# Performance work log

Hardware: AMD Instinct MI355X
Metric: run time of the kernel (lower is better)

The kernel has to match this reference:

```python
import jax, jax.numpy as jnp
import numpy as np
import math

NUM_HEADS = 16
ATTN_WIDTH = 256


def setup_inputs() -> dict:
    key = jax.random.key(0)
    ks = jax.random.split(key, 5)
    B, S, C, H = 2, 2048, 1024, 1024
    scale = 0.02
    return {
        "x": jax.random.normal(ks[0], (B, S, C), dtype=jnp.float32),
        "Wq": jax.random.normal(ks[1], (C, H), dtype=jnp.float32) * scale,
        "Wk": jax.random.normal(ks[2], (C, H), dtype=jnp.float32) * scale,
        "Wv": jax.random.normal(ks[3], (C, H), dtype=jnp.float32) * scale,
        "Wo": jax.random.normal(ks[4], (H, C), dtype=jnp.float32) * scale,
    }


def reference(x, Wq, Wk, Wv, Wo):
    B, S, C = x.shape
    H = NUM_HEADS
    dh = Wq.shape[1] // H  # head dim; Q.size(-1) in torch code

    def split_heads(t):
        # [B, S, H*dh] -> [B, H, S, dh]
        return t.reshape(B, S, H, dh).transpose(0, 2, 1, 3)

    q = split_heads(x @ Wq)
    k = split_heads(x @ Wk)
    v = split_heads(x @ Wv)

    scores = jnp.einsum("bhqd,bhkd->bhqk", q, k) / math.sqrt(dh)
    # exp-shift (first 'softmax-like' step, unnormalized)
    scores = jnp.exp(scores - jnp.max(scores, axis=-1, keepdims=True))
    # banded mask: tril(attn_width//2 - 1).triu(-(attn_width//2))
    i = jnp.arange(S)[:, None]
    j = jnp.arange(S)[None, :]
    d = j - i
    half = ATTN_WIDTH // 2
    mask = (d <= half - 1) & (d >= -half)
    scores = jnp.where(mask, scores, 0.0)
    # second softmax over the masked exp-scores (zeros contribute exp(0)=1)
    weights = jax.nn.softmax(scores, axis=-1)

    out = jnp.einsum("bhqk,bhkd->bhqd", weights, v)  # [B, H, S, dh]
    out = out.transpose(0, 2, 1, 3).reshape(B, S, H * dh)
    return out @ Wo
```

## Files before the change

kernel.cpp:

```cpp
#include <hip/hip_runtime.h>
#include <math.h>

typedef __bf16 bf16_t;
typedef bf16_t bf16x8 __attribute__((ext_vector_type(8)));
typedef bf16_t bf16x4 __attribute__((ext_vector_type(4)));
typedef float f32x4 __attribute__((ext_vector_type(4)));

constexpr int S_ = 2048;
constexpr float SCALE = 0.125f;

#define MFMA_B16(a, b, c) __builtin_amdgcn_mfma_f32_16x16x32_bf16(a, b, c, 0, 0, 0)

#define WAIT_VM0() __builtin_amdgcn_s_waitcnt(0x0F70)
#define WAIT_VM4() __builtin_amdgcn_s_waitcnt(0x0F74)
#define WAIT_VM8() __builtin_amdgcn_s_waitcnt(0x0F78)
#define BARRIER()  __builtin_amdgcn_s_barrier()

typedef __attribute__((address_space(1))) const void* as1_cvp;
typedef __attribute__((address_space(3))) void* as3_vp;

__device__ __forceinline__ void gl2lds16(const void* g, void* l)
{
    __builtin_amdgcn_global_load_lds((as1_cvp)g, (as3_vp)l, 16, 0, 0);
}

__global__ __launch_bounds__(256) void prep(const float* __restrict__ x,
                                            const float* __restrict__ Wq,
                                            const float* __restrict__ Wk,
                                            const float* __restrict__ Wv,
                                            const float* __restrict__ Wo,
                                            bf16_t* __restrict__ xb,
                                            bf16_t* __restrict__ Wqt,
                                            bf16_t* __restrict__ Wkt,
                                            bf16_t* __restrict__ Wvt,
                                            bf16_t* __restrict__ Wot,
                                            float* __restrict__ vsp)
{
    __shared__ float T[64][65];
    const int blk = blockIdx.x;
    const int tid = threadIdx.x;
    if (blk < 1024) {
#pragma unroll
        for (int u = 0; u < 4; ++u) {
            const int g = blk * 1024 + u * 256 + tid;
            const float4 v = ((const float4*)x)[g];
            bf16x4 o;
            o[0] = (bf16_t)v.x; o[1] = (bf16_t)v.y;
            o[2] = (bf16_t)v.z; o[3] = (bf16_t)v.w;
            *(bf16x4*)&xb[(size_t)g * 4] = o;
        }
    } else if (blk < 2048) {
        const int rem = blk - 1024;
        const int wsel = rem >> 8, t = rem & 255;
        const float* src = (wsel == 0) ? Wq : (wsel == 1) ? Wk : (wsel == 2) ? Wv : Wo;
        bf16_t* dst = (wsel == 0) ? Wqt : (wsel == 1) ? Wkt : (wsel == 2) ? Wvt : Wot;
        const int k0 = (t >> 4) * 64, n0 = (t & 15) * 64;
        const int rr = tid >> 4, c4 = (tid & 15) * 4;
#pragma unroll
        for (int u = 0; u < 4; ++u) {
            const float4 v = *(const float4*)&src[(size_t)(k0 + u * 16 + rr) * 1024 + n0 + c4];
            T[u * 16 + rr][c4 + 0] = v.x; T[u * 16 + rr][c4 + 1] = v.y;
            T[u * 16 + rr][c4 + 2] = v.z; T[u * 16 + rr][c4 + 3] = v.w;
        }
        __syncthreads();
#pragma unroll
        for (int u = 0; u < 4; ++u) {
            bf16x4 o;
#pragma unroll
            for (int e = 0; e < 4; ++e) o[e] = (bf16_t)T[c4 + e][u * 16 + rr];
            *(bf16x4*)&dst[(size_t)(n0 + u * 16 + rr) * 1024 + k0 + c4] = o;
        }
    } else {
#pragma unroll
        for (int u = 0; u < 8; ++u) vsp[u * 256 + tid] = 0.f;
    }
}

template <int MODE>
__device__ __forceinline__ void mfma_gemm_body(const bf16_t* __restrict__ A,
                                               const bf16_t* __restrict__ Bt,
                                               void* __restrict__ dst,
                                               float* __restrict__ vsum_out,
                                               int m0, int n0)
{
    __shared__ bf16_t As[12288];
    __shared__ bf16_t Bs[12288];

    const int tid = threadIdx.x;
    const int lane = tid & 63, wid = tid >> 6;
    const int l15 = lane & 15, quad = lane >> 4;
    const int wm = (wid & 1) * 64, wn = (wid >> 1) * 64;

    const int srow = wid * 32 + (lane >> 2);
    const int scg8 = (lane & 3) * 8;
    const bf16_t* Ag0 = A  + (size_t)(m0 + srow) * 1024 + scg8;
    const bf16_t* Ag1 = A  + (size_t)(m0 + srow + 16) * 1024 + scg8;
    const bf16_t* Bg0 = Bt + (size_t)(n0 + srow) * 1024 + scg8;
    const bf16_t* Bg1 = Bt + (size_t)(n0 + srow + 16) * 1024 + scg8;

    f32x4 acc[4][4];
#pragma unroll
    for (int i = 0; i < 4; ++i)
#pragma unroll
        for (int j = 0; j < 4; ++j) acc[i][j] = (f32x4){0.f, 0.f, 0.f, 0.f};

#pragma unroll
    for (int p = 0; p < 2; ++p) {
        const int k0 = p * 32;
        gl2lds16(Ag0 + k0, As + p * 4096 + (wid * 2 + 0) * 512);
        gl2lds16(Ag1 + k0, As + p * 4096 + (wid * 2 + 1) * 512);
        gl2lds16(Bg0 + k0, Bs + p * 4096 + (wid * 2 + 0) * 512);
        gl2lds16(Bg1 + k0, Bs + p * 4096 + (wid * 2 + 1) * 512);
    }

    int cbuf = 0, sbuf = 2;
    for (int it = 0; it < 32; ++it) {
        if (it + 2 < 32) WAIT_VM4(); else WAIT_VM0();
        BARRIER();
        if (it + 2 < 32) {
            const int k0 = (it + 2) * 32;
            gl2lds16(Ag0 + k0, As + sbuf * 4096 + (wid * 2 + 0) * 512);
            gl2lds16(Ag1 + k0, As + sbuf * 4096 + (wid * 2 + 1) * 512);
            gl2lds16(Bg0 + k0, Bs + sbuf * 4096 + (wid * 2 + 0) * 512);
            gl2lds16(Bg1 + k0, Bs + sbuf * 4096 + (wid * 2 + 1) * 512);
            sbuf = (sbuf == 2) ? 0 : sbuf + 1;
        }
        bf16x8 af[4], bfr[4];
#pragma unroll
        for (int mt = 0; mt < 4; ++mt)
            af[mt] = *(const bf16x8*)&As[cbuf * 4096 + (wm + mt * 16 + l15) * 32 + quad * 8];
#pragma unroll
        for (int nt = 0; nt < 4; ++nt)
            bfr[nt] = *(const bf16x8*)&Bs[cbuf * 4096 + (wn + nt * 16 + l15) * 32 + quad * 8];
#pragma unroll
        for (int mt = 0; mt < 4; ++mt)
#pragma unroll
            for (int nt = 0; nt < 4; ++nt)
                acc[mt][nt] = MFMA_B16(bfr[nt], af[mt], acc[mt][nt]);
        cbuf = (cbuf == 2) ? 0 : cbuf + 1;
    }

#pragma unroll
    for (int mt = 0; mt < 4; ++mt) {
        const int m = m0 + wm + mt * 16 + l15;
#pragma unroll
        for (int nt = 0; nt < 4; ++nt) {
            const int nb = n0 + wn + nt * 16 + quad * 4;
            if (MODE == 0) {
                *(f32x4*)&((float*)dst)[(size_t)m * 1024 + nb] = acc[mt][nt];
            } else {
                const int bb = m >> 11, s = m & 2047;
                const int hh = nb >> 6, d = nb & 63;
                bf16x4 o;
#pragma unroll
                for (int u = 0; u < 4; ++u) o[u] = (bf16_t)acc[mt][nt][u];
                *(bf16x4*)&((bf16_t*)dst)[((size_t)(bb * 16 + hh) * 2048 + s) * 64 + d] = o;
            }
        }
    }

    if (MODE == 1 && vsum_out != nullptr) {
        const int bb = m0 >> 11;
#pragma unroll
        for (int nt = 0; nt < 4; ++nt) {
            f32x4 p = acc[0][nt];
#pragma unroll
            for (int mt = 1; mt < 4; ++mt) {
                p[0] += acc[mt][nt][0]; p[1] += acc[mt][nt][1];
                p[2] += acc[mt][nt][2]; p[3] += acc[mt][nt][3];
            }
#pragma unroll
            for (int st = 1; st < 16; st <<= 1) {
                p[0] += __shfl_xor(p[0], st);
                p[1] += __shfl_xor(p[1], st);
                p[2] += __shfl_xor(p[2], st);
                p[3] += __shfl_xor(p[3], st);
            }
            if (l15 == 0) {
                const int nI = n0 + wn + nt * 16 + quad * 4;
                float* vp = &vsum_out[(bb * 16 + (nI >> 6)) * 64 + (nI & 63)];
                atomicAdd(vp + 0, p[0]);
                atomicAdd(vp + 1, p[1]);
                atomicAdd(vp + 2, p[2]);
                atomicAdd(vp + 3, p[3]);
            }
        }
    }
}

__global__ __launch_bounds__(256) void gemm_qkv_mfma(const bf16_t* __restrict__ xb,
                                                     const bf16_t* __restrict__ Wqt,
                                                     const bf16_t* __restrict__ Wkt,
                                                     const bf16_t* __restrict__ Wvt,
                                                     bf16_t* Qh, bf16_t* Kh, bf16_t* Vh,
                                                     float* vsp)
{
    const bf16_t* Bt = (blockIdx.z == 0) ? Wqt : (blockIdx.z == 1) ? Wkt : Wvt;
    bf16_t* dst = (blockIdx.z == 0) ? Qh : (blockIdx.z == 1) ? Kh : Vh;
    float* vs = (blockIdx.z == 2) ? vsp : nullptr;
    mfma_gemm_body<1>(xb, Bt, dst, vs, blockIdx.y * 128, blockIdx.x * 128);
}

__global__ __launch_bounds__(256) void gemm_out_mfma(const bf16_t* __restrict__ attn,
                                                     const bf16_t* __restrict__ Wot,
                                                     float* __restrict__ out)
{
    mfma_gemm_body<0>(attn, Wot, out, nullptr, blockIdx.y * 128, blockIdx.x * 128);
}

__global__ __launch_bounds__(256) void attn_fused(const bf16_t* __restrict__ Qh,
                                                  const bf16_t* __restrict__ Kh,
                                                  const bf16_t* __restrict__ Vh,
                                                  const float* __restrict__ vsp,
                                                  bf16_t* __restrict__ attn)
{
    __shared__ bf16_t Qs[8192];
    __shared__ bf16_t Kp[24576];
    __shared__ float msh[4][8][16];
    float (*zsh)[32] = (float(*)[32])msh;

    bf16_t* Ks2 = Kp;
    bf16_t* Vt  = Kp + 4096;
    bf16_t* Ws  = Kp + 8704;

    const int tid = threadIdx.x;
    const int lane = tid & 63, wid = tid >> 6;
    const int l15 = lane & 15, quad = lane >> 4;

    const int f = blockIdx.x;
    const int seq = f >> 3;
    const int bh = (f & 7) + 8 * (seq >> 4);
    const int i0 = (seq & 15) * 128;
    const int b = bh >> 4, h = bh & 15;
    const bf16_t* Qb = Qh + (size_t)bh * 131072;
    const bf16_t* Kb = Kh + (size_t)bh * 131072;
    const bf16_t* Vb = Vh + (size_t)bh * 131072;

#pragma unroll
    for (int c = 0; c < 4; ++c) {
        const int g = wid * 4 + c;
        const int half = g >> 3;
        const int row = (g & 7) * 16 + (lane >> 2);
        gl2lds16(Qb + (size_t)(i0 + row) * 64 + half * 32 + (lane & 3) * 8,
                 Qs + g * 512);
    }
#pragma unroll
    for (int p = 0; p < 2; ++p) {
#pragma unroll
        for (int c = 0; c < 4; ++c) {
            const int g = wid * 4 + c;
            const int half = g >> 3;
            const int row = (g & 7) * 16 + (lane >> 2);
            gl2lds16(Kb + (size_t)(p * 128 + row) * 64 + half * 32 + (lane & 3) * 8,
                     Kp + p * 8192 + g * 512);
        }
    }
    WAIT_VM8();
    BARRIER();

    bf16x8 af[8][2];
#pragma unroll
    for (int mt = 0; mt < 8; ++mt)
#pragma unroll
        for (int ks = 0; ks < 2; ++ks)
            af[mt][ks] = *(const bf16x8*)&Qs[ks * 4096 + (mt * 16 + l15) * 32 + quad * 8];

    float rmax[8];
#pragma unroll
    for (int mt = 0; mt < 8; ++mt) rmax[mt] = -3.0e38f;

    int cbuf = 0, sbuf = 2;
    for (int jc = 0; jc < 16; ++jc) {
        if (jc + 2 < 16) WAIT_VM4(); else WAIT_VM0();
        BARRIER();
        if (jc + 2 < 16) {
            bf16_t* nb = Kp + sbuf * 8192;
#pragma unroll
            for (int c = 0; c < 4; ++c) {
                const int g = wid * 4 + c;
                const int half = g >> 3;
                const int row = (g & 7) * 16 + (lane >> 2);
                gl2lds16(Kb + (size_t)((jc + 2) * 128 + row) * 64 + half * 32 + (lane & 3) * 8,
                         nb + g * 512);
            }
            sbuf = (sbuf == 2) ? 0 : sbuf + 1;
        }
        const bf16_t* cb = Kp + cbuf * 8192;
#pragma unroll
        for (int ntl = 0; ntl < 2; ++ntl) {
            const int jt = wid * 2 + ntl;
            const bf16x8 b0 = *(const bf16x8*)&cb[(jt * 16 + l15) * 32 + quad * 8];
            const bf16x8 b1 = *(const bf16x8*)&cb[4096 + (jt * 16 + l15) * 32 + quad * 8];
#pragma unroll
            for (int mt = 0; mt < 8; ++mt) {
                f32x4 t = (f32x4){0.f, 0.f, 0.f, 0.f};
                t = MFMA_B16(b0, af[mt][0], t);
                t = MFMA_B16(b1, af[mt][1], t);
                rmax[mt] = fmaxf(rmax[mt], fmaxf(fmaxf(t[0], t[1]), fmaxf(t[2], t[3])));
            }
        }
        cbuf = (cbuf == 2) ? 0 : cbuf + 1;
    }
#pragma unroll
    for (int mt = 0; mt < 8; ++mt) {
        float v = rmax[mt];
        v = fmaxf(v, __shfl_xor(v, 16));
        v = fmaxf(v, __shfl_xor(v, 32));
        if (quad == 0) msh[wid][mt][l15] = v;
    }
    __syncthreads();

    float mreg[2][4];
#pragma unroll
    for (int t = 0; t < 2; ++t)
#pragma unroll
        for (int r = 0; r < 4; ++r) {
            const int mt = wid * 2 + t;
            const int il = quad * 4 + r;
            mreg[t][r] = SCALE * fmaxf(fmaxf(msh[0][mt][il], msh[1][mt][il]),
                                       fmaxf(msh[2][mt][il], msh[3][mt][il]));
        }

    f32x4 vsd4[4];
#pragma unroll
    for (int dt = 0; dt < 4; ++dt)
        vsd4[dt] = *(const f32x4*)&vsp[bh * 64 + dt * 16 + quad * 4];

    f32x4 accO[2][4];
#pragma unroll
    for (int t = 0; t < 2; ++t)
#pragma unroll
        for (int dt = 0; dt < 4; ++dt) accO[t][dt] = (f32x4){0.f, 0.f, 0.f, 0.f};
    float zp[2][4] = {{0.f, 0.f, 0.f, 0.f}, {0.f, 0.f, 0.f, 0.f}};

    for (int cb2 = 0; cb2 < 6; ++cb2) {
        const int jb = i0 - 128 + cb2 * 64;
        if (jb < 0 || jb >= S_) continue;

        __syncthreads();
#pragma unroll
        for (int c = 0; c < 2; ++c) {
            const int g = wid * 2 + c;
            const int half = g >> 2;
            const int row = (g & 3) * 16 + (lane >> 2);
            gl2lds16(Kb + (size_t)(jb + row) * 64 + half * 32 + (lane & 3) * 8,
                     Ks2 + g * 512);
        }
        {
            const bf16x8 v0 = *(const bf16x8*)&Vb[(size_t)(jb + lane) * 64 + wid * 16];
            const bf16x8 v1 = *(const bf16x8*)&Vb[(size_t)(jb + lane) * 64 + wid * 16 + 8];
#pragma unroll
            for (int e = 0; e < 8; ++e) {
                Vt[(wid * 16 + e) * 72 + lane] = v0[e];
                Vt[(wid * 16 + 8 + e) * 72 + lane] = v1[e];
            }
        }
        __syncthreads();

#pragma unroll
        for (int t = 0; t < 2; ++t) {
            const int mt = wid * 2 + t;
#pragma unroll
            for (int jt4 = 0; jt4 < 4; ++jt4) {
                const bf16x8 k0 = *(const bf16x8*)&Ks2[(jt4 * 16 + l15) * 32 + quad * 8];
                const bf16x8 k1 = *(const bf16x8*)&Ks2[2048 + (jt4 * 16 + l15) * 32 + quad * 8];
                f32x4 sc = (f32x4){0.f, 0.f, 0.f, 0.f};
                sc = MFMA_B16(af[mt][0], k0, sc);
                sc = MFMA_B16(af[mt][1], k1, sc);
#pragma unroll
                for (int r = 0; r < 4; ++r) {
                    const int ig = i0 + mt * 16 + quad * 4 + r;
                    const int jg = jb + jt4 * 16 + l15;
                    const int dd = jg - ig;
                    const bool ok = (dd >= -128) && (dd <= 127);
                    const float e1 = __expf(sc[r] * SCALE - mreg[t][r]);
                    const float wv = ok ? (__expf(e1) - 1.0f) : 0.0f;
                    const bf16_t wb = (bf16_t)wv;
                    zp[t][r] += (float)wb;
                    Ws[(mt * 16 + quad * 4 + r) * 72 + jt4 * 16 + l15] = wb;
                }
            }
        }
        __syncthreads();

#pragma unroll
        for (int ks = 0; ks < 2; ++ks) {
            bf16x8 bv[4];
#pragma unroll
            for (int dt = 0; dt < 4; ++dt)
                bv[dt] = *(const bf16x8*)&Vt[(dt * 16 + l15) * 72 + ks * 32 + quad * 8];
#pragma unroll
            for (int t = 0; t < 2; ++t) {
                const int mt = wid * 2 + t;
                const bf16x8 aw = *(const bf16x8*)&Ws[(mt * 16 + l15) * 72 + ks * 32 + quad * 8];
#pragma unroll
                for (int dt = 0; dt < 4; ++dt)
                    accO[t][dt] = MFMA_B16(bv[dt], aw, accO[t][dt]);
            }
        }
    }

#pragma unroll
    for (int t = 0; t < 2; ++t)
#pragma unroll
        for (int r = 0; r < 4; ++r) {
            float z = zp[t][r];
            z += __shfl_xor(z, 1);
            z += __shfl_xor(z, 2);
            z += __shfl_xor(z, 4);
            z += __shfl_xor(z, 8);
            if (l15 == 0) zsh[wid][t * 16 + quad * 4 + r] = z + (float)S_;
        }
    __syncthreads();

#pragma unroll
    for (int t = 0; t < 2; ++t) {
        const float rz = 1.0f / zsh[wid][t * 16 + l15];
        const int irow = i0 + (wid * 2 + t) * 16 + l15;
#pragma unroll
        for (int dt = 0; dt < 4; ++dt) {
            bf16x4 o;
#pragma unroll
            for (int r = 0; r < 4; ++r)
                o[r] = (bf16_t)((accO[t][dt][r] + vsd4[dt][r]) * rz);
            *(bf16x4*)&attn[(size_t)(b * S_ + irow) * 1024 + h * 64 + dt * 16 + quad * 4] = o;
        }
    }
}

extern "C" void kernel_launch(void* const* d_in, const int* in_sizes, int n_in,
                              void* d_out, int out_size, void* d_ws, size_t ws_size,
                              hipStream_t stream)
{
    const float* x  = (const float*)d_in[0];
    const float* Wq = (const float*)d_in[1];
    const float* Wk = (const float*)d_in[2];
    const float* Wv = (const float*)d_in[3];
    const float* Wo = (const float*)d_in[4];
    float* out = (float*)d_out;

    char* ws = (char*)d_ws;
    bf16_t* xb   = (bf16_t*)(ws + 0);
    bf16_t* Wqt  = (bf16_t*)(ws + 8388608);
    bf16_t* Wkt  = (bf16_t*)(ws + 10485760);
    bf16_t* Wvt  = (bf16_t*)(ws + 12582912);
    bf16_t* Wot  = (bf16_t*)(ws + 14680064);
    bf16_t* Qh   = (bf16_t*)(ws + 16777216);
    bf16_t* Kh   = (bf16_t*)(ws + 25165824);
    bf16_t* Vh   = (bf16_t*)(ws + 33554432);
    bf16_t* attn = (bf16_t*)(ws + 41943040);
    float*  vsp  = (float*)(ws + 50331648);

    prep<<<2049, 256, 0, stream>>>(x, Wq, Wk, Wv, Wo, xb, Wqt, Wkt, Wvt, Wot, vsp);
    gemm_qkv_mfma<<<dim3(8, 32, 3), 256, 0, stream>>>(xb, Wqt, Wkt, Wvt, Qh, Kh, Vh, vsp);
    attn_fused<<<512, 256, 0, stream>>>(Qh, Kh, Vh, vsp, attn);
    gemm_out_mfma<<<dim3(8, 32), 256, 0, stream>>>(attn, Wot, out);
}
```

Before: 190.0 us.

## Split fused attention into separate row-max and banded softmax-PV kernels

The fused attention kernel is split in two. A rowmax kernel computes the full-row score maximum, and a band kernel does the banded exp/softmax and the PV product using a precomputed per-row max from global memory. The aim is to reduce register and LDS pressure in each kernel so occupancy rises. The new rowmax kernel drops the triple-buffered async K prefetch for a single buffer with syncthreads, which may expose load latency. The GEMM k-loop is also fully unrolled with compile-time buffer indices, which adds one extra launch and a small global round trip.

```diff
diff --git a/kernel.cpp b/kernel.cpp
--- a/kernel.cpp
+++ b/kernel.cpp
@@ -13,7 +13,6 @@
 
 #define WAIT_VM0() __builtin_amdgcn_s_waitcnt(0x0F70)
 #define WAIT_VM4() __builtin_amdgcn_s_waitcnt(0x0F74)
-#define WAIT_VM8() __builtin_amdgcn_s_waitcnt(0x0F78)
 #define BARRIER()  __builtin_amdgcn_s_barrier()
 
 typedef __attribute__((address_space(1))) const void* as1_cvp;
@@ -113,31 +112,31 @@
         gl2lds16(Bg1 + k0, Bs + p * 4096 + (wid * 2 + 1) * 512);
     }
 
-    int cbuf = 0, sbuf = 2;
+#pragma unroll
     for (int it = 0; it < 32; ++it) {
-        if (it + 2 < 32) WAIT_VM4(); else WAIT_VM0();
+        if (it < 30) WAIT_VM4(); else WAIT_VM0();
         BARRIER();
-        if (it + 2 < 32) {
+        if (it < 30) {
             const int k0 = (it + 2) * 32;
-            gl2lds16(Ag0 + k0, As + sbuf * 4096 + (wid * 2 + 0) * 512);
-            gl2lds16(Ag1 + k0, As + sbuf * 4096 + (wid * 2 + 1) * 512);
-            gl2lds16(Bg0 + k0, Bs + sbuf * 4096 + (wid * 2 + 0) * 512);
-            gl2lds16(Bg1 + k0, Bs + sbuf * 4096 + (wid * 2 + 1) * 512);
-            sbuf = (sbuf == 2) ? 0 : sbuf + 1;
-        }
+            const int sb = (it + 2) % 3;
+            gl2lds16(Ag0 + k0, As + sb * 4096 + (wid * 2 + 0) * 512);
+            gl2lds16(Ag1 + k0, As + sb * 4096 + (wid * 2 + 1) * 512);
+            gl2lds16(Bg0 + k0, Bs + sb * 4096 + (wid * 2 + 0) * 512);
+            gl2lds16(Bg1 + k0, Bs + sb * 4096 + (wid * 2 + 1) * 512);
+        }
+        const int cb = it % 3;
         bf16x8 af[4], bfr[4];
 #pragma unroll
         for (int mt = 0; mt < 4; ++mt)
-            af[mt] = *(const bf16x8*)&As[cbuf * 4096 + (wm + mt * 16 + l15) * 32 + quad * 8];
+            af[mt] = *(const bf16x8*)&As[cb * 4096 + (wm + mt * 16 + l15) * 32 + quad * 8];
 #pragma unroll
         for (int nt = 0; nt < 4; ++nt)
-            bfr[nt] = *(const bf16x8*)&Bs[cbuf * 4096 + (wn + nt * 16 + l15) * 32 + quad * 8];
+            bfr[nt] = *(const bf16x8*)&Bs[cb * 4096 + (wn + nt * 16 + l15) * 32 + quad * 8];
 #pragma unroll
         for (int mt = 0; mt < 4; ++mt)
 #pragma unroll
             for (int nt = 0; nt < 4; ++nt)
                 acc[mt][nt] = MFMA_B16(bfr[nt], af[mt], acc[mt][nt]);
-        cbuf = (cbuf == 2) ? 0 : cbuf + 1;
     }
 
 #pragma unroll
@@ -208,20 +207,106 @@
     mfma_gemm_body<0>(attn, Wot, out, nullptr, blockIdx.y * 128, blockIdx.x * 128);
 }
 
-__global__ __launch_bounds__(256) void attn_fused(const bf16_t* __restrict__ Qh,
-                                                  const bf16_t* __restrict__ Kh,
-                                                  const bf16_t* __restrict__ Vh,
-                                                  const float* __restrict__ vsp,
-                                                  bf16_t* __restrict__ attn)
+__global__ __launch_bounds__(256) void rowmax_k(const bf16_t* __restrict__ Qh,
+                                                const bf16_t* __restrict__ Kh,
+                                                float* __restrict__ mrow)
 {
     __shared__ bf16_t Qs[8192];
-    __shared__ bf16_t Kp[24576];
+    __shared__ bf16_t Ks[8192];
     __shared__ float msh[4][8][16];
-    float (*zsh)[32] = (float(*)[32])msh;
-
-    bf16_t* Ks2 = Kp;
-    bf16_t* Vt  = Kp + 4096;
-    bf16_t* Ws  = Kp + 8704;
+
+    const int tid = threadIdx.x;
+    const int lane = tid & 63, wid = tid >> 6;
+    const int l15 = lane & 15, quad = lane >> 4;
+
+    const int f = blockIdx.x;
+    const int seq = f >> 3;
+    const int bh = (f & 7) + 8 * (seq >> 4);
+    const int i0 = (seq & 15) * 128;
+    const bf16_t* Qb = Qh + (size_t)bh * 131072;
+    const bf16_t* Kb = Kh + (size_t)bh * 131072;
+
+#pragma unroll
+    for (int c = 0; c < 4; ++c) {
+        const int g = wid * 4 + c;
+        const int half = g >> 3;
+        const int row = (g & 7) * 16 + (lane >> 2);
+        gl2lds16(Qb + (size_t)(i0 + row) * 64 + half * 32 + (lane & 3) * 8,
+                 Qs + g * 512);
+    }
+    __syncthreads();
+
+    bf16x8 af[8][2];
+#pragma unroll
+    for (int mt = 0; mt < 8; ++mt)
+#pragma unroll
+        for (int ks = 0; ks < 2; ++ks)
+            af[mt][ks] = *(const bf16x8*)&Qs[ks * 4096 + (mt * 16 + l15) * 32 + quad * 8];
+
+    f32x4 vm[8];
+#pragma unroll
+    for (int mt = 0; mt < 8; ++mt)
+        vm[mt] = (f32x4){-3.0e38f, -3.0e38f, -3.0e38f, -3.0e38f};
+
+    for (int jc = 0; jc < 16; ++jc) {
+        __syncthreads();
+#pragma unroll
+        for (int c = 0; c < 4; ++c) {
+            const int g = wid * 4 + c;
+            const int half = g >> 3;
+            const int row = (g & 7) * 16 + (lane >> 2);
+            gl2lds16(Kb + (size_t)(jc * 128 + row) * 64 + half * 32 + (lane & 3) * 8,
+                     Ks + g * 512);
+        }
+        __syncthreads();
+
+#pragma unroll
+        for (int ntl = 0; ntl < 2; ++ntl) {
+            const int jt = wid * 2 + ntl;
+            const bf16x8 b0 = *(const bf16x8*)&Ks[(jt * 16 + l15) * 32 + quad * 8];
+            const bf16x8 b1 = *(const bf16x8*)&Ks[4096 + (jt * 16 + l15) * 32 + quad * 8];
+#pragma unroll
+            for (int mt = 0; mt < 8; ++mt) {
+                f32x4 t = (f32x4){0.f, 0.f, 0.f, 0.f};
+                t = MFMA_B16(b0, af[mt][0], t);
+                t = MFMA_B16(b1, af[mt][1], t);
+                vm[mt][0] = fmaxf(vm[mt][0], t[0]);
+                vm[mt][1] = fmaxf(vm[mt][1], t[1]);
+                vm[mt][2] = fmaxf(vm[mt][2], t[2]);
+                vm[mt][3] = fmaxf(vm[mt][3], t[3]);
+            }
+        }
+    }
+
+#pragma unroll
+    for (int mt = 0; mt < 8; ++mt) {
+        float v = fmaxf(fmaxf(vm[mt][0], vm[mt][1]), fmaxf(vm[mt][2], vm[mt][3]));
+        v = fmaxf(v, __shfl_xor(v, 16));
+        v = fmaxf(v, __shfl_xor(v, 32));
+        if (quad == 0) msh[wid][mt][l15] = v;
+    }
+    __syncthreads();
+
+    if (tid < 128) {
+        const int mt = tid >> 4, il = tid & 15;
+        const float v = fmaxf(fmaxf(msh[0][mt][il], msh[1][mt][il]),
+                              fmaxf(msh[2][mt][il], msh[3][mt][il]));
+        mrow[(size_t)bh * S_ + i0 + mt * 16 + il] = v * SCALE;
+    }
+}
+
+__global__ __launch_bounds__(256) void band_k(const bf16_t* __restrict__ Qh,
+                                              const bf16_t* __restrict__ Kh,
+                                              const bf16_t* __restrict__ Vh,
+                                              const float* __restrict__ mrow,
+                                              const float* __restrict__ vsp,
+                                              bf16_t* __restrict__ attn)
+{
+    __shared__ bf16_t Qs[8192];
+    __shared__ bf16_t Ks2[4096];
+    __shared__ bf16_t Vt[4608];
+    __shared__ bf16_t Ws[9216];
+    __shared__ float zsh[4][32];
 
     const int tid = threadIdx.x;
     const int lane = tid & 63, wid = tid >> 6;
@@ -244,82 +329,21 @@
         gl2lds16(Qb + (size_t)(i0 + row) * 64 + half * 32 + (lane & 3) * 8,
                  Qs + g * 512);
     }
-#pragma unroll
-    for (int p = 0; p < 2; ++p) {
-#pragma unroll
-        for (int c = 0; c < 4; ++c) {
-            const int g = wid * 4 + c;
-            const int half = g >> 3;
-            const int row = (g & 7) * 16 + (lane >> 2);
-            gl2lds16(Kb + (size_t)(p * 128 + row) * 64 + half * 32 + (lane & 3) * 8,
-                     Kp + p * 8192 + g * 512);
-        }
-    }
-    WAIT_VM8();
-    BARRIER();
-
-    bf16x8 af[8][2];
-#pragma unroll
-    for (int mt = 0; mt < 8; ++mt)
+    __syncthreads();
+
+    bf16x8 aq[2][2];
+#pragma unroll
+    for (int t = 0; t < 2; ++t)
 #pragma unroll
         for (int ks = 0; ks < 2; ++ks)
-            af[mt][ks] = *(const bf16x8*)&Qs[ks * 4096 + (mt * 16 + l15) * 32 + quad * 8];
-
-    float rmax[8];
-#pragma unroll
-    for (int mt = 0; mt < 8; ++mt) rmax[mt] = -3.0e38f;
-
-    int cbuf = 0, sbuf = 2;
-    for (int jc = 0; jc < 16; ++jc) {
-        if (jc + 2 < 16) WAIT_VM4(); else WAIT_VM0();
-        BARRIER();
-        if (jc + 2 < 16) {
-            bf16_t* nb = Kp + sbuf * 8192;
-#pragma unroll
-            for (int c = 0; c < 4; ++c) {
-                const int g = wid * 4 + c;
-                const int half = g >> 3;
-                const int row = (g & 7) * 16 + (lane >> 2);
-                gl2lds16(Kb + (size_t)((jc + 2) * 128 + row) * 64 + half * 32 + (lane & 3) * 8,
-                         nb + g * 512);
-            }
-            sbuf = (sbuf == 2) ? 0 : sbuf + 1;
-        }
-        const bf16_t* cb = Kp + cbuf * 8192;
-#pragma unroll
-        for (int ntl = 0; ntl < 2; ++ntl) {
-            const int jt = wid * 2 + ntl;
-            const bf16x8 b0 = *(const bf16x8*)&cb[(jt * 16 + l15) * 32 + quad * 8];
-            const bf16x8 b1 = *(const bf16x8*)&cb[4096 + (jt * 16 + l15) * 32 + quad * 8];
-#pragma unroll
-            for (int mt = 0; mt < 8; ++mt) {
-                f32x4 t = (f32x4){0.f, 0.f, 0.f, 0.f};
-                t = MFMA_B16(b0, af[mt][0], t);
-                t = MFMA_B16(b1, af[mt][1], t);
-                rmax[mt] = fmaxf(rmax[mt], fmaxf(fmaxf(t[0], t[1]), fmaxf(t[2], t[3])));
-            }
-        }
-        cbuf = (cbuf == 2) ? 0 : cbuf + 1;
-    }
-#pragma unroll
-    for (int mt = 0; mt < 8; ++mt) {
-        float v = rmax[mt];
-        v = fmaxf(v, __shfl_xor(v, 16));
-        v = fmaxf(v, __shfl_xor(v, 32));
-        if (quad == 0) msh[wid][mt][l15] = v;
-    }
-    __syncthreads();
+            aq[t][ks] = *(const bf16x8*)&Qs[ks * 4096 + ((wid * 2 + t) * 16 + l15) * 32 + quad * 8];
 
     float mreg[2][4];
 #pragma unroll
     for (int t = 0; t < 2; ++t)
 #pragma unroll
-        for (int r = 0; r < 4; ++r) {
-            const int mt = wid * 2 + t;
-            const int il = quad * 4 + r;
-            mreg[t][r] = SCALE * fmaxf(fmaxf(msh[0][mt][il], msh[1][mt][il]),
-                                       fmaxf(msh[2][mt][il], msh[3][mt][il]));
-        }
+        for (int r = 0; r < 4; ++r)
+            mreg[t][r] = mrow[(size_t)bh * S_ + i0 + (wid * 2 + t) * 16 + quad * 4 + r];
 
     f32x4 vsd4[4];
 #pragma unroll
@@ -365,8 +389,8 @@
                 const bf16x8 k0 = *(const bf16x8*)&Ks2[(jt4 * 16 + l15) * 32 + quad * 8];
                 const bf16x8 k1 = *(const bf16x8*)&Ks2[2048 + (jt4 * 16 + l15) * 32 + quad * 8];
                 f32x4 sc = (f32x4){0.f, 0.f, 0.f, 0.f};
-                sc = MFMA_B16(af[mt][0], k0, sc);
-                sc = MFMA_B16(af[mt][1], k1, sc);
+                sc = MFMA_B16(aq[t][0], k0, sc);
+                sc = MFMA_B16(aq[t][1], k1, sc);
 #pragma unroll
                 for (int r = 0; r < 4; ++r) {
                     const int ig = i0 + mt * 16 + quad * 4 + r;
@@ -450,9 +474,11 @@
     bf16_t* Vh   = (bf16_t*)(ws + 33554432);
     bf16_t* attn = (bf16_t*)(ws + 41943040);
     float*  vsp  = (float*)(ws + 50331648);
+    float*  mrow = (float*)(ws + 50339840);
 
     prep<<<2049, 256, 0, stream>>>(x, Wq, Wk, Wv, Wo, xb, Wqt, Wkt, Wvt, Wot, vsp);
     gemm_qkv_mfma<<<dim3(8, 32, 3), 256, 0, stream>>>(xb, Wqt, Wkt, Wvt, Qh, Kh, Vh, vsp);
-    attn_fused<<<512, 256, 0, stream>>>(Qh, Kh, Vh, vsp, attn);
+    rowmax_k<<<512, 256, 0, stream>>>(Qh, Kh, mrow);
+    band_k<<<512, 256, 0, stream>>>(Qh, Kh, Vh, mrow, vsp, attn);
     gemm_out_mfma<<<dim3(8, 32), 256, 0, stream>>>(attn, Wot, out);
 }
```

Result: no change. 187.9 us (-1.1%).
